# Performance work log

Measured on AMD Instinct MI355X. Metric: run time of the kernel, lower is better.

The kernel has to match this reference:

```python
import jax, jax.numpy as jnp
import numpy as np

B, N = 1, 768
C_S, C_Z, C_H, H, PQ, PV = 384, 128, 16, 12, 4, 8
INF, EPS = 1e5, 1e-8
SOFTPLUS_INV_1 = 0.541324854612918


def _quat_to_rot(q):
    # q: [..., 4] unit quaternions (w, x, y, z) -> [..., 3, 3]
    w, x, y, z = q[..., 0], q[..., 1], q[..., 2], q[..., 3]
    R = jnp.stack([
        1 - 2 * (y * y + z * z), 2 * (x * y - w * z), 2 * (x * z + w * y),
        2 * (x * y + w * z), 1 - 2 * (x * x + z * z), 2 * (y * z - w * x),
        2 * (x * z - w * y), 2 * (y * z + w * x), 1 - 2 * (x * x + y * y),
    ], axis=-1)
    return R.reshape(q.shape[:-1] + (3, 3))


def setup_inputs() -> dict:
    key = jax.random.key(0)
    ks = jax.random.split(key, 24)
    def lin(k, din, dout):
        return jax.random.normal(k, (din, dout), jnp.float32) / np.sqrt(din)
    quat = jax.random.normal(ks[2], (B, N, 4), jnp.float32)
    quat = quat / jnp.linalg.norm(quat, axis=-1, keepdims=True)
    return {
        "s": jax.random.normal(ks[0], (B, N, C_S), jnp.float32),
        "z": jax.random.normal(ks[1], (B, N, N, C_Z), jnp.float32),
        "rot": _quat_to_rot(quat),
        "trans": 10.0 * jax.random.normal(ks[3], (B, N, 3), jnp.float32),
        "mask": jnp.ones((B, N), jnp.float32),
        "wq": lin(ks[4], C_S, H * C_H), "bq": jnp.zeros((H * C_H,), jnp.float32),
        "wkv": lin(ks[5], C_S, 2 * H * C_H), "bkv": jnp.zeros((2 * H * C_H,), jnp.float32),
        "wqp": lin(ks[6], C_S, H * PQ * 3), "bqp": jnp.zeros((H * PQ * 3,), jnp.float32),
        "wkvp": lin(ks[7], C_S, H * (PQ + PV) * 3), "bkvp": jnp.zeros((H * (PQ + PV) * 3,), jnp.float32),
        "wb": lin(ks[8], C_Z, H), "bb": jnp.zeros((H,), jnp.float32),
        "wdz": lin(ks[9], C_Z, C_Z // 4), "bdz": jnp.zeros((C_Z // 4,), jnp.float32),
        "head_weights": jnp.full((H,), SOFTPLUS_INV_1, jnp.float32),
        "wout": lin(ks[10], H * (C_Z // 4 + C_H + PV * 4), C_S),
        "bout": jnp.zeros((C_S,), jnp.float32),
    }


def reference(s, z, rot, trans, mask, wq, bq, wkv, bkv, wqp, bqp, wkvp, bkvp,
              wb, bb, wdz, bdz, head_weights, wout, bout):
    # scalar q, k, v: [B, N, H, C_H]
    q = (s @ wq + bq).reshape(B, N, H, C_H)
    kv = (s @ wkv + bkv).reshape(B, N, H, 2 * C_H)
    k, v = kv[..., :C_H], kv[..., C_H:]

    def make_pts(w, b, npts):
        p = s @ w + b                                       # [B, N, H*npts*3]
        p = jnp.stack(jnp.split(p, 3, axis=-1), axis=-1)    # [B, N, H*npts, 3]
        p = jnp.einsum('bnxy,bnpy->bnpx', rot, p) + trans[:, :, None, :]
        return p.reshape(B, N, H, npts, 3)

    q_pts = make_pts(wqp, bqp, PQ)                          # [B, N, H, PQ, 3]
    kv_pts = make_pts(wkvp, bkvp, PQ + PV)
    k_pts, v_pts = kv_pts[..., :PQ, :], kv_pts[..., PQ:, :]

    b_bias = z @ wb + bb                                    # [B, N, N, H]
    a = jnp.einsum('bihc,bjhc->bhij', q, k) * np.sqrt(1.0 / (3 * C_H))
    a = a + np.sqrt(1.0 / 3) * jnp.transpose(b_bias, (0, 3, 1, 2))

    disp = q_pts[:, :, None] - k_pts[:, None]               # [B, i, j, H, PQ, 3]
    pt_att = jnp.sum(disp ** 2, axis=-1)                    # [B, i, j, H, PQ]
    hw = jax.nn.softplus(head_weights) * np.sqrt(1.0 / (3 * (PQ * 9.0 / 2)))
    pt_att = -0.5 * jnp.sum(pt_att * hw[:, None], axis=-1)  # [B, i, j, H]
    a = a + jnp.transpose(pt_att, (0, 3, 1, 2))

    sq_mask = INF * (mask[:, :, None] * mask[:, None, :] - 1.0)
    a = jax.nn.softmax(a + sq_mask[:, None], axis=-1)       # [B, H, i, j]

    o = jnp.einsum('bhij,bjhc->bihc', a, v).reshape(B, N, -1)
    o_pt = jnp.einsum('bhij,bjhpx->bihpx', a, v_pts)        # [B, N, H, PV, 3]
    o_pt = jnp.einsum('bixy,bihpx->bihpy', rot, o_pt - trans[:, :, None, None, :])
    o_pt_norm = jnp.sqrt(jnp.sum(o_pt ** 2, axis=-1) + EPS).reshape(B, N, -1)
    o_pt = o_pt.reshape(B, N, -1, 3)

    pair_z = z @ wdz + bdz                                  # [B, N, N, C_Z//4]
    o_pair = jnp.einsum('bhij,bijc->bihc', a, pair_z).reshape(B, N, -1)

    feats = jnp.concatenate(
        [o, o_pt[..., 0], o_pt[..., 1], o_pt[..., 2], o_pt_norm, o_pair], axis=-1)
    return feats @ wout + bout
```

## Files before the change

kernel.cpp:

```cpp
#include <hip/hip_runtime.h>
#include <hip/hip_bf16.h>
#include <math.h>

#define NTOK 768
#define CS   384
#define CZ   128
#define NH   12
#define INF_ 100000.0f
#define EPS_ 1e-8f

typedef unsigned int  uint32;
typedef __attribute__((ext_vector_type(8))) short bf16x8;
typedef __attribute__((ext_vector_type(4))) float f32x4;

__device__ __forceinline__ float bflo(uint32 u) { return __uint_as_float((u & 0xffffu) << 16); }
__device__ __forceinline__ float bfhi(uint32 u) { return __uint_as_float(u & 0xffff0000u); }
__device__ __forceinline__ uint32 pkbf(float a, float b) {
    union { unsigned short s[2]; uint32 u; } r;
    __hip_bfloat16 ha = __float2bfloat16(a);
    __hip_bfloat16 hb = __float2bfloat16(b);
    __builtin_memcpy(&r.s[0], &ha, 2);
    __builtin_memcpy(&r.s[1], &hb, 2);
    return r.u;
}

#define QK_SCALE 0.14433756729740643f
#define B_SCALE  0.5773502691896258f
#define HW_SCALE 0.13608276348795434f

__global__ __launch_bounds__(256) void k1a_gemm(
    const float* __restrict__ s,
    const float* __restrict__ wq, const float* __restrict__ wkv,
    const float* __restrict__ wqp, const float* __restrict__ wkvp,
    float* __restrict__ RAW)
{
    __shared__ float sA[32][72];
    __shared__ float sB[32][72];
    const int tid  = threadIdx.x;
    const int tok0 = blockIdx.x * 64;
    const int col0 = blockIdx.y * 64;

    const int m0 = (tid & 15) * 4;
    const int n0 = (tid >> 4) * 4;

    float4 acc[4];
    #pragma unroll
    for (int nn = 0; nn < 4; nn++) acc[nn] = make_float4(0.f, 0.f, 0.f, 0.f);

    const int lam = tid >> 2, lak = (tid & 3) * 8;
    const int lbk = tid >> 3, lbc = (tid & 7) * 8;
    const int gcol = col0 + lbc;
    const float* wsrc; int wwidth, woff;
    if (gcol < 192)      { wsrc = wq;   wwidth = 192; woff = gcol; }
    else if (gcol < 576) { wsrc = wkv;  wwidth = 384; woff = gcol - 192; }
    else if (gcol < 720) { wsrc = wqp;  wwidth = 144; woff = gcol - 576; }
    else                 { wsrc = wkvp; wwidth = 432; woff = gcol - 720; }

    for (int kb = 0; kb < CS; kb += 32) {
        const float4 a0 = *(const float4*)&s[(tok0 + lam) * CS + kb + lak];
        const float4 a1 = *(const float4*)&s[(tok0 + lam) * CS + kb + lak + 4];
        const float4 b0 = *(const float4*)&wsrc[(size_t)(kb + lbk) * wwidth + woff];
        const float4 b1 = *(const float4*)&wsrc[(size_t)(kb + lbk) * wwidth + woff + 4];
        __syncthreads();
        sA[lak + 0][lam] = a0.x; sA[lak + 1][lam] = a0.y;
        sA[lak + 2][lam] = a0.z; sA[lak + 3][lam] = a0.w;
        sA[lak + 4][lam] = a1.x; sA[lak + 5][lam] = a1.y;
        sA[lak + 6][lam] = a1.z; sA[lak + 7][lam] = a1.w;
        *(float4*)&sB[lbk][lbc]     = b0;
        *(float4*)&sB[lbk][lbc + 4] = b1;
        __syncthreads();
        #pragma unroll
        for (int k = 0; k < 32; k++) {
            const float4 av = *(const float4*)&sA[k][m0];
            const float4 bv = *(const float4*)&sB[k][n0];
            acc[0].x += av.x * bv.x; acc[0].y += av.y * bv.x; acc[0].z += av.z * bv.x; acc[0].w += av.w * bv.x;
            acc[1].x += av.x * bv.y; acc[1].y += av.y * bv.y; acc[1].z += av.z * bv.y; acc[1].w += av.w * bv.y;
            acc[2].x += av.x * bv.z; acc[2].y += av.y * bv.z; acc[2].z += av.z * bv.z; acc[2].w += av.w * bv.z;
            acc[3].x += av.x * bv.w; acc[3].y += av.y * bv.w; acc[3].z += av.z * bv.w; acc[3].w += av.w * bv.w;
        }
    }
    #pragma unroll
    for (int nn = 0; nn < 4; nn++)
        *(float4*)&RAW[(size_t)(col0 + n0 + nn) * NTOK + tok0 + m0] = acc[nn];
}

__global__ __launch_bounds__(256) void k1b_finish(
    const float* __restrict__ RAW,
    const float* __restrict__ rot, const float* __restrict__ trans,
    const float* __restrict__ bq, const float* __restrict__ bkv,
    const float* __restrict__ bqp, const float* __restrict__ bkvp,
    const float* __restrict__ head_weights,
    float* __restrict__ VT, float* __restrict__ QP, float* __restrict__ VPT,
    float* __restrict__ AP, float* __restrict__ BP,
    float* __restrict__ RQN, float* __restrict__ CKN)
{
    __shared__ float hwS[NH];
    const int tid = threadIdx.x;
    const int t  = blockIdx.x * 16 + (tid & 15);
    const int wk = tid >> 4;

    if (tid < NH) hwS[tid] = logf(1.0f + expf(head_weights[tid])) * HW_SCALE;

    float R[9], T3[3];
    #pragma unroll
    for (int x = 0; x < 9; x++) R[x] = rot[t * 9 + x];
    #pragma unroll
    for (int x = 0; x < 3; x++) T3[x] = trans[t * 3 + x];
    __syncthreads();

    for (int col = wk; col < 192; col += 16) {
        const int h = col >> 4, c = col & 15;
        AP[(size_t)(h * 28 + c) * NTOK + t] = QK_SCALE * (RAW[(size_t)col * NTOK + t] + bq[col]);
    }
    for (int idx = wk; idx < 192; idx += 16) {
        const int h = idx >> 4, c = idx & 15;
        BP[(size_t)(h * 28 + c) * NTOK + t] = RAW[(size_t)(192 + h * 32 + c) * NTOK + t] + bkv[h * 32 + c];
        VT[idx * NTOK + t] = RAW[(size_t)(192 + h * 32 + 16 + c) * NTOK + t] + bkv[h * 32 + 16 + c];
    }
    for (int pidx = wk; pidx < 48; pidx += 16) {
        const int h = pidx >> 2, p = pidx & 3;
        const float r0 = RAW[(size_t)(576 + 0 * 48 + pidx) * NTOK + t] + bqp[0 * 48 + pidx];
        const float r1 = RAW[(size_t)(576 + 1 * 48 + pidx) * NTOK + t] + bqp[1 * 48 + pidx];
        const float r2 = RAW[(size_t)(576 + 2 * 48 + pidx) * NTOK + t] + bqp[2 * 48 + pidx];
        #pragma unroll
        for (int x = 0; x < 3; x++) {
            const float v = R[x*3+0]*r0 + R[x*3+1]*r1 + R[x*3+2]*r2 + T3[x];
            QP[t * 144 + pidx * 3 + x] = v;
            AP[(size_t)(h * 28 + 16 + p * 3 + x) * NTOK + t] = hwS[h] * v;
        }
    }
    for (int pidx = wk; pidx < 144; pidx += 16) {
        const int h = pidx / 12, pp = pidx % 12;
        const float r0 = RAW[(size_t)(720 + 0 * 144 + pidx) * NTOK + t] + bkvp[0 * 144 + pidx];
        const float r1 = RAW[(size_t)(720 + 1 * 144 + pidx) * NTOK + t] + bkvp[1 * 144 + pidx];
        const float r2 = RAW[(size_t)(720 + 2 * 144 + pidx) * NTOK + t] + bkvp[2 * 144 + pidx];
        #pragma unroll
        for (int x = 0; x < 3; x++) {
            const float v = R[x*3+0]*r0 + R[x*3+1]*r1 + R[x*3+2]*r2 + T3[x];
            if (pp < 4) BP[(size_t)(h * 28 + 16 + pp * 3 + x) * NTOK + t] = v;
            else        VPT[((h * 8 + pp - 4) * 3 + x) * NTOK + t] = v;
        }
    }
    __syncthreads();
    if (wk < NH) {
        const int h = wk;
        float sq = 0.f, sk = 0.f;
        #pragma unroll
        for (int d = 0; d < 12; d++) {
            const float a = QP[t * 144 + h * 12 + d];
            sq += a * a;
            const float b = BP[(size_t)(h * 28 + 16 + d) * NTOK + t];
            sk += b * b;
        }
        RQN[h * NTOK + t] = -0.5f * hwS[h] * sq;
        CKN[h * NTOK + t] = -0.5f * hwS[h] * sk;
    }
}

__global__ __launch_bounds__(256) void k2_zproj_mfma(
    const float* __restrict__ z, const float* __restrict__ wb, const float* __restrict__ bb,
    const float* __restrict__ wdz, const float* __restrict__ bdz,
    float* __restrict__ BBT, uint32* __restrict__ PZB)
{
    __shared__ __align__(16) unsigned short wB[48 * 136];
    __shared__ float outS[2][64][53];
    __shared__ float bbS[12], bdzS[32];

    const int tid = threadIdx.x;
    const int i   = blockIdx.x;
    const int l   = tid & 63;
    const int jt  = tid >> 6;

    for (int idx = tid; idx < 48 * 64; idx += 256) {
        const int o = idx >> 6, k2 = (idx & 63) * 2;
        float f0, f1;
        if (o < 12)      { f0 = wb[k2 * 12 + o];         f1 = wb[(k2 + 1) * 12 + o]; }
        else if (o < 44) { f0 = wdz[k2 * 32 + (o - 12)]; f1 = wdz[(k2 + 1) * 32 + (o - 12)]; }
        else             { f0 = 0.f; f1 = 0.f; }
        *(uint32*)&wB[o * 136 + k2] = pkbf(f0, f1);
    }
    if (tid < 12) bbS[tid] = bb[tid];
    else if (tid >= 32 && tid < 64) bdzS[tid - 32] = bdz[tid - 32];
    __syncthreads();

    bf16x8 Bf[3][4];
    #pragma unroll
    for (int t = 0; t < 3; t++)
        #pragma unroll
        for (int ks = 0; ks < 4; ks++)
            Bf[t][ks] = *(const bf16x8*)&wB[(t * 16 + (l & 15)) * 136 + ks * 32 + (l >> 4) * 8];

    const float* zb = z + ((size_t)i * NTOK + jt * 16 + (l & 15)) * CZ + (l >> 4) * 8;

    float4 pa[8];
    #pragma unroll
    for (int ks = 0; ks < 4; ks++) {
        pa[2 * ks]     = *(const float4*)&zb[ks * 32];
        pa[2 * ks + 1] = *(const float4*)&zb[ks * 32 + 4];
    }

    for (int tile = 0; tile < 12; tile++) {
        const int j0  = tile * 64;
        const int buf = tile & 1;

        union { uint32 u[4]; bf16x8 v; } Au[4];
        #pragma unroll
        for (int ks = 0; ks < 4; ks++) {
            Au[ks].u[0] = pkbf(pa[2 * ks].x,     pa[2 * ks].y);
            Au[ks].u[1] = pkbf(pa[2 * ks].z,     pa[2 * ks].w);
            Au[ks].u[2] = pkbf(pa[2 * ks + 1].x, pa[2 * ks + 1].y);
            Au[ks].u[3] = pkbf(pa[2 * ks + 1].z, pa[2 * ks + 1].w);
        }
        if (tile < 11) {
            const float* zn = zb + (size_t)(tile + 1) * 64 * CZ;
            #pragma unroll
            for (int ks = 0; ks < 4; ks++) {
                pa[2 * ks]     = *(const float4*)&zn[ks * 32];
                pa[2 * ks + 1] = *(const float4*)&zn[ks * 32 + 4];
            }
        }

        f32x4 acc[3];
        #pragma unroll
        for (int t = 0; t < 3; t++) acc[t] = (f32x4){0.f, 0.f, 0.f, 0.f};
        #pragma unroll
        for (int ks = 0; ks < 4; ks++)
            #pragma unroll
            for (int t = 0; t < 3; t++)
                acc[t] = __builtin_amdgcn_mfma_f32_16x16x32_bf16(Au[ks].v, Bf[t][ks], acc[t], 0, 0, 0);

        #pragma unroll
        for (int t = 0; t < 3; t++) {
            const int o = t * 16 + (l & 15);
            #pragma unroll
            for (int v = 0; v < 4; v++)
                outS[buf][jt * 16 + (l >> 4) * 4 + v][o] = acc[t][v];
        }
        __syncthreads();

        for (int idx = tid; idx < 12 * 64; idx += 256) {
            const int o = idx >> 6, jl = idx & 63;
            BBT[((size_t)i * 12 + o) * NTOK + j0 + jl] = outS[buf][jl][o] + bbS[o];
        }
        for (int idx = tid; idx < 32 * 32; idx += 256) {
            const int c = idx >> 5, jp = idx & 31;
            const float f0 = outS[buf][jp * 2][12 + c] + bdzS[c];
            const float f1 = outS[buf][jp * 2 + 1][12 + c] + bdzS[c];
            PZB[(size_t)(i * 32 + c) * 384 + (j0 >> 1) + jp] = pkbf(f0, f1);
        }
    }
}

__global__ __launch_bounds__(768) void k3_fused(
    const float* __restrict__ AP, const float* __restrict__ BP,
    const float* __restrict__ RQN, const float* __restrict__ CKN,
    const float* __restrict__ BBT, const float* __restrict__ mask,
    const float* __restrict__ VT, const float* __restrict__ VPT,
    const uint32* __restrict__ PZB,
    float* __restrict__ O, float* __restrict__ OPT, float* __restrict__ OPAIR)
{
    const int i = blockIdx.x, tid = threadIdx.x;
    const int h = tid >> 6, l = tid & 63;

    float ap[28];
    #pragma unroll
    for (int k = 0; k < 28; k++) ap[k] = AP[(size_t)(h * 28 + k) * NTOK + i];
    const float rq = RQN[h * NTOK + i];
    const float mi = mask[i];

    f32x4 lg[3];
    #pragma unroll
    for (int qb = 0; qb < 3; qb++) {
        const int j4 = qb * 256 + l * 4;
        const float4 ck  = *(const float4*)&CKN[h * NTOK + j4];
        const float4 bbv = *(const float4*)&BBT[((size_t)i * 12 + h) * NTOK + j4];
        const float4 mj  = *(const float4*)&mask[j4];
        f32x4 a;
        a[0] = B_SCALE * bbv.x + rq + ck.x + INF_ * (mi * mj.x - 1.0f);
        a[1] = B_SCALE * bbv.y + rq + ck.y + INF_ * (mi * mj.y - 1.0f);
        a[2] = B_SCALE * bbv.z + rq + ck.z + INF_ * (mi * mj.z - 1.0f);
        a[3] = B_SCALE * bbv.w + rq + ck.w + INF_ * (mi * mj.w - 1.0f);
        #pragma unroll
        for (int k = 0; k < 28; k++) {
            const float4 bp = *(const float4*)&BP[(size_t)(h * 28 + k) * NTOK + j4];
            a[0] += ap[k] * bp.x; a[1] += ap[k] * bp.y;
            a[2] += ap[k] * bp.z; a[3] += ap[k] * bp.w;
        }
        lg[qb] = a;
    }

    float m = -3.0e38f;
    #pragma unroll
    for (int qb = 0; qb < 3; qb++)
        #pragma unroll
        for (int v = 0; v < 4; v++) m = fmaxf(m, lg[qb][v]);
    #pragma unroll
    for (int off = 32; off >= 1; off >>= 1) m = fmaxf(m, __shfl_xor(m, off));
    float ssum = 0.0f;
    #pragma unroll
    for (int qb = 0; qb < 3; qb++)
        #pragma unroll
        for (int v = 0; v < 4; v++) {
            const float e = __expf(lg[qb][v] - m);
            lg[qb][v] = e;
            ssum += e;
        }
    #pragma unroll
    for (int off = 32; off >= 1; off >>= 1) ssum += __shfl_xor(ssum, off);
    const float inv = 1.0f / ssum;
    #pragma unroll
    for (int qb = 0; qb < 3; qb++)
        #pragma unroll
        for (int v = 0; v < 4; v++) lg[qb][v] *= inv;

    #pragma unroll 2
    for (int r = 0; r < 40; r++) {
        const float4* src = (r < 16) ? (const float4*)&VT[(h * 16 + r) * NTOK]
                                     : (const float4*)&VPT[(h * 24 + (r - 16)) * NTOK];
        const float4 v0 = src[l], v1 = src[64 + l], v2 = src[128 + l];
        float acc = lg[0][0]*v0.x + lg[0][1]*v0.y + lg[0][2]*v0.z + lg[0][3]*v0.w
                  + lg[1][0]*v1.x + lg[1][1]*v1.y + lg[1][2]*v1.z + lg[1][3]*v1.w
                  + lg[2][0]*v2.x + lg[2][1]*v2.y + lg[2][2]*v2.z + lg[2][3]*v2.w;
        #pragma unroll
        for (int off = 32; off >= 1; off >>= 1) acc += __shfl_xor(acc, off);
        if (l == 0) {
            if (r < 16) O[i * 192 + h * 16 + r] = acc;
            else        OPT[i * 288 + h * 24 + (r - 16)] = acc;
        }
    }
    #pragma unroll 2
    for (int c = 0; c < 32; c++) {
        const uint2* src = (const uint2*)PZB + (size_t)(i * 32 + c) * 192;
        float a = 0.f;
        #pragma unroll
        for (int it = 0; it < 3; it++) {
            const uint2 u = src[it * 64 + l];
            a += lg[it][0] * bflo(u.x) + lg[it][1] * bfhi(u.x)
               + lg[it][2] * bflo(u.y) + lg[it][3] * bfhi(u.y);
        }
        #pragma unroll
        for (int off = 32; off >= 1; off >>= 1) a += __shfl_xor(a, off);
        if (l == 0) OPAIR[i * 384 + h * 32 + c] = a;
    }
}

#define K4T 8
__global__ __launch_bounds__(256) void k4_out(
    const float* __restrict__ O, const float* __restrict__ OPT, const float* __restrict__ OPAIR,
    const float* __restrict__ rot, const float* __restrict__ trans,
    const float* __restrict__ wout, const float* __restrict__ bout,
    float* __restrict__ out)
{
    __shared__ float f[K4T][960];
    const int n0 = blockIdx.x * K4T, tid = threadIdx.x;

    for (int idx = tid; idx < K4T * 192; idx += 256) {
        const int t = idx / 192, k = idx % 192;
        f[t][k] = O[(n0 + t) * 192 + k];
    }
    for (int idx = tid; idx < K4T * 384; idx += 256) {
        const int t = idx / 384, k = idx % 384;
        f[t][576 + k] = OPAIR[(n0 + t) * 384 + k];
    }
    for (int idx = tid; idx < K4T * 96; idx += 256) {
        const int t = idx / 96, hp = idx % 96;
        const int n = n0 + t;
        const float vx = OPT[n * 288 + hp * 3 + 0] - trans[n * 3 + 0];
        const float vy = OPT[n * 288 + hp * 3 + 1] - trans[n * 3 + 1];
        const float vz = OPT[n * 288 + hp * 3 + 2] - trans[n * 3 + 2];
        const float o0 = rot[n*9+0]*vx + rot[n*9+3]*vy + rot[n*9+6]*vz;
        const float o1 = rot[n*9+1]*vx + rot[n*9+4]*vy + rot[n*9+7]*vz;
        const float o2 = rot[n*9+2]*vx + rot[n*9+5]*vy + rot[n*9+8]*vz;
        f[t][192 + hp] = o0;
        f[t][288 + hp] = o1;
        f[t][384 + hp] = o2;
        f[t][480 + hp] = sqrtf(o0*o0 + o1*o1 + o2*o2 + EPS_);
    }
    __syncthreads();

    for (int o = tid; o < 384; o += 256) {
        float acc[K4T];
        #pragma unroll
        for (int t = 0; t < K4T; t++) acc[t] = bout[o];
        for (int kq = 0; kq < 240; kq++) {
            float4 fv[K4T];
            #pragma unroll
            for (int t = 0; t < K4T; t++) fv[t] = *(const float4*)&f[t][kq * 4];
            #pragma unroll
            for (int kk = 0; kk < 4; kk++) {
                const float wv = wout[(kq * 4 + kk) * 384 + o];
                #pragma unroll
                for (int t = 0; t < K4T; t++) {
                    const float fe = (kk == 0) ? fv[t].x : (kk == 1) ? fv[t].y
                                   : (kk == 2) ? fv[t].z : fv[t].w;
                    acc[t] += fe * wv;
                }
            }
        }
        #pragma unroll
        for (int t = 0; t < K4T; t++) out[(n0 + t) * 384 + o] = acc[t];
    }
}

extern "C" void kernel_launch(void* const* d_in, const int* in_sizes, int n_in,
                              void* d_out, int out_size, void* d_ws, size_t ws_size,
                              hipStream_t stream) {
    (void)in_sizes; (void)n_in; (void)out_size; (void)ws_size;
    const float* s     = (const float*)d_in[0];
    const float* z     = (const float*)d_in[1];
    const float* rot   = (const float*)d_in[2];
    const float* trans = (const float*)d_in[3];
    const float* mask  = (const float*)d_in[4];
    const float* wq    = (const float*)d_in[5];
    const float* bq    = (const float*)d_in[6];
    const float* wkv   = (const float*)d_in[7];
    const float* bkv   = (const float*)d_in[8];
    const float* wqp   = (const float*)d_in[9];
    const float* bqp   = (const float*)d_in[10];
    const float* wkvp  = (const float*)d_in[11];
    const float* bkvp  = (const float*)d_in[12];
    const float* wb    = (const float*)d_in[13];
    const float* bb    = (const float*)d_in[14];
    const float* wdz   = (const float*)d_in[15];
    const float* bdz   = (const float*)d_in[16];
    const float* hwts  = (const float*)d_in[17];
    const float* wout  = (const float*)d_in[18];
    const float* bout  = (const float*)d_in[19];
    float* out = (float*)d_out;

    float* ws = (float*)d_ws;
    float* Q     = ws;
    float* KT    = Q     + 147456;
    float* VT    = KT    + 147456;
    float* QP    = VT    + 147456;
    float* KPT   = QP    + 110592;
    float* VPT   = KPT   + 110592;
    float* O     = VPT   + 221184;
    float* OPT   = O     + 147456;
    float* OPAIR = OPT   + 221184;
    float* BBT   = OPAIR + 294912;
    uint32* PZB  = (uint32*)(BBT + 7077888);
    float* AP    = BBT + 7077888 + 9437184;
    float* BP    = AP  + 258048;
    float* RQN   = BP  + 258048;
    float* CKN   = RQN + 9216;
    float* RAW = BBT;

    hipLaunchKernelGGL(k1a_gemm, dim3(NTOK / 64, 1152 / 64), dim3(256), 0, stream,
                       s, wq, wkv, wqp, wkvp, RAW);
    hipLaunchKernelGGL(k1b_finish, dim3(NTOK / 16), dim3(256), 0, stream,
                       RAW, rot, trans, bq, bkv, bqp, bkvp, hwts,
                       VT, QP, VPT, AP, BP, RQN, CKN);
    hipLaunchKernelGGL(k2_zproj_mfma, dim3(NTOK), dim3(256), 0, stream,
                       z, wb, bb, wdz, bdz, BBT, PZB);
    hipLaunchKernelGGL(k3_fused, dim3(NTOK), dim3(768), 0, stream,
                       AP, BP, RQN, CKN, BBT, mask, VT, VPT, PZB,
                       O, OPT, OPAIR);
    hipLaunchKernelGGL(k4_out, dim3(NTOK / K4T), dim3(256), 0, stream,
                       O, OPT, OPAIR, rot, trans, wout, bout, out);
}
```

Before: 383.9 us.

## Fuse z-projection into attention kernel, keeping pair bias and pair values in LDS

New measurement: 329.0 us. 1.17x faster.

```diff
diff --git a/kernel.cpp b/kernel.cpp
--- a/kernel.cpp
+++ b/kernel.cpp
@@ -157,27 +157,31 @@
     }
 }
 
-__global__ __launch_bounds__(256) void k2_zproj_mfma(
+__global__ __launch_bounds__(768) void k23_fused(
     const float* __restrict__ z, const float* __restrict__ wb, const float* __restrict__ bb,
     const float* __restrict__ wdz, const float* __restrict__ bdz,
-    float* __restrict__ BBT, uint32* __restrict__ PZB)
+    const float* __restrict__ AP, const float* __restrict__ BP,
+    const float* __restrict__ RQN, const float* __restrict__ CKN,
+    const float* __restrict__ mask,
+    const float* __restrict__ VT, const float* __restrict__ VPT,
+    float* __restrict__ O, float* __restrict__ OPT, float* __restrict__ OPAIR)
 {
-    __shared__ __align__(16) unsigned short wB[48 * 136];
-    __shared__ float outS[2][64][53];
+    __shared__ __align__(16) unsigned short wBs[48 * 136];
+    __shared__ float  bbL[12][772];
+    __shared__ uint32 pzL[32][386];
     __shared__ float bbS[12], bdzS[32];
 
-    const int tid = threadIdx.x;
-    const int i   = blockIdx.x;
-    const int l   = tid & 63;
-    const int jt  = tid >> 6;
-
-    for (int idx = tid; idx < 48 * 64; idx += 256) {
+    const int i = blockIdx.x, tid = threadIdx.x;
+    const int h = tid >> 6;
+    const int l = tid & 63;
+
+    for (int idx = tid; idx < 48 * 64; idx += 768) {
         const int o = idx >> 6, k2 = (idx & 63) * 2;
         float f0, f1;
         if (o < 12)      { f0 = wb[k2 * 12 + o];         f1 = wb[(k2 + 1) * 12 + o]; }
         else if (o < 44) { f0 = wdz[k2 * 32 + (o - 12)]; f1 = wdz[(k2 + 1) * 32 + (o - 12)]; }
         else             { f0 = 0.f; f1 = 0.f; }
-        *(uint32*)&wB[o * 136 + k2] = pkbf(f0, f1);
+        *(uint32*)&wBs[o * 136 + k2] = pkbf(f0, f1);
     }
     if (tid < 12) bbS[tid] = bb[tid];
     else if (tid >= 32 && tid < 64) bdzS[tid - 32] = bdz[tid - 32];
@@ -188,10 +192,9 @@
     for (int t = 0; t < 3; t++)
         #pragma unroll
         for (int ks = 0; ks < 4; ks++)
-            Bf[t][ks] = *(const bf16x8*)&wB[(t * 16 + (l & 15)) * 136 + ks * 32 + (l >> 4) * 8];
-
-    const float* zb = z + ((size_t)i * NTOK + jt * 16 + (l & 15)) * CZ + (l >> 4) * 8;
-
+            Bf[t][ks] = *(const bf16x8*)&wBs[(t * 16 + (l & 15)) * 136 + ks * 32 + (l >> 4) * 8];
+
+    const float* zb = z + ((size_t)i * NTOK + h * 64 + (l & 15)) * CZ + (l >> 4) * 8;
     float4 pa[8];
     #pragma unroll
     for (int ks = 0; ks < 4; ks++) {
@@ -199,10 +202,9 @@
         pa[2 * ks + 1] = *(const float4*)&zb[ks * 32 + 4];
     }
 
-    for (int tile = 0; tile < 12; tile++) {
-        const int j0  = tile * 64;
-        const int buf = tile & 1;
-
+    #pragma unroll
+    for (int st = 0; st < 4; st++) {
+        const int jb = h * 64 + st * 16;
         union { uint32 u[4]; bf16x8 v; } Au[4];
         #pragma unroll
         for (int ks = 0; ks < 4; ks++) {
@@ -211,8 +213,8 @@
             Au[ks].u[2] = pkbf(pa[2 * ks + 1].x, pa[2 * ks + 1].y);
             Au[ks].u[3] = pkbf(pa[2 * ks + 1].z, pa[2 * ks + 1].w);
         }
-        if (tile < 11) {
-            const float* zn = zb + (size_t)(tile + 1) * 64 * CZ;
+        if (st < 3) {
+            const float* zn = zb + (size_t)(st + 1) * 16 * CZ;
             #pragma unroll
             for (int ks = 0; ks < 4; ks++) {
                 pa[2 * ks]     = *(const float4*)&zn[ks * 32];
@@ -229,38 +231,23 @@
             for (int t = 0; t < 3; t++)
                 acc[t] = __builtin_amdgcn_mfma_f32_16x16x32_bf16(Au[ks].v, Bf[t][ks], acc[t], 0, 0, 0);
 
+        const int jq = jb + (l >> 4) * 4;
         #pragma unroll
         for (int t = 0; t < 3; t++) {
             const int o = t * 16 + (l & 15);
-            #pragma unroll
-            for (int v = 0; v < 4; v++)
-                outS[buf][jt * 16 + (l >> 4) * 4 + v][o] = acc[t][v];
-        }
-        __syncthreads();
-
-        for (int idx = tid; idx < 12 * 64; idx += 256) {
-            const int o = idx >> 6, jl = idx & 63;
-            BBT[((size_t)i * 12 + o) * NTOK + j0 + jl] = outS[buf][jl][o] + bbS[o];
-        }
-        for (int idx = tid; idx < 32 * 32; idx += 256) {
-            const int c = idx >> 5, jp = idx & 31;
-            const float f0 = outS[buf][jp * 2][12 + c] + bdzS[c];
-            const float f1 = outS[buf][jp * 2 + 1][12 + c] + bdzS[c];
-            PZB[(size_t)(i * 32 + c) * 384 + (j0 >> 1) + jp] = pkbf(f0, f1);
-        }
-    }
-}
-
-__global__ __launch_bounds__(768) void k3_fused(
-    const float* __restrict__ AP, const float* __restrict__ BP,
-    const float* __restrict__ RQN, const float* __restrict__ CKN,
-    const float* __restrict__ BBT, const float* __restrict__ mask,
-    const float* __restrict__ VT, const float* __restrict__ VPT,
-    const uint32* __restrict__ PZB,
-    float* __restrict__ O, float* __restrict__ OPT, float* __restrict__ OPAIR)
-{
-    const int i = blockIdx.x, tid = threadIdx.x;
-    const int h = tid >> 6, l = tid & 63;
+            if (o < 12) {
+                #pragma unroll
+                for (int v = 0; v < 4; v++)
+                    bbL[o][jq + v] = acc[t][v] + bbS[o];
+            } else if (o < 44) {
+                const int c = o - 12;
+                const float bz = bdzS[c];
+                pzL[c][(jq >> 1)]     = pkbf(acc[t][0] + bz, acc[t][1] + bz);
+                pzL[c][(jq >> 1) + 1] = pkbf(acc[t][2] + bz, acc[t][3] + bz);
+            }
+        }
+    }
+    __syncthreads();
 
     float ap[28];
     #pragma unroll
@@ -273,7 +260,7 @@
     for (int qb = 0; qb < 3; qb++) {
         const int j4 = qb * 256 + l * 4;
         const float4 ck  = *(const float4*)&CKN[h * NTOK + j4];
-        const float4 bbv = *(const float4*)&BBT[((size_t)i * 12 + h) * NTOK + j4];
+        const float4 bbv = *(const float4*)&bbL[h][j4];
         const float4 mj  = *(const float4*)&mask[j4];
         f32x4 a;
         a[0] = B_SCALE * bbv.x + rq + ck.x + INF_ * (mi * mj.x - 1.0f);
@@ -330,13 +317,13 @@
     }
     #pragma unroll 2
     for (int c = 0; c < 32; c++) {
-        const uint2* src = (const uint2*)PZB + (size_t)(i * 32 + c) * 192;
         float a = 0.f;
         #pragma unroll
         for (int it = 0; it < 3; it++) {
-            const uint2 u = src[it * 64 + l];
-            a += lg[it][0] * bflo(u.x) + lg[it][1] * bfhi(u.x)
-               + lg[it][2] * bflo(u.y) + lg[it][3] * bfhi(u.y);
+            const uint32* p2 = &pzL[c][it * 128 + 2 * l];
+            const uint32 ux = p2[0], uy = p2[1];
+            a += lg[it][0] * bflo(ux) + lg[it][1] * bfhi(ux)
+               + lg[it][2] * bflo(uy) + lg[it][3] * bfhi(uy);
         }
         #pragma unroll
         for (int off = 32; off >= 1; off >>= 1) a += __shfl_xor(a, off);
@@ -438,23 +425,20 @@
     float* O     = VPT   + 221184;
     float* OPT   = O     + 147456;
     float* OPAIR = OPT   + 221184;
-    float* BBT   = OPAIR + 294912;
-    uint32* PZB  = (uint32*)(BBT + 7077888);
-    float* AP    = BBT + 7077888 + 9437184;
+    float* RAW   = OPAIR + 294912;
+    float* AP    = RAW   + 884736;
     float* BP    = AP  + 258048;
     float* RQN   = BP  + 258048;
     float* CKN   = RQN + 9216;
-    float* RAW = BBT;
 
     hipLaunchKernelGGL(k1a_gemm, dim3(NTOK / 64, 1152 / 64), dim3(256), 0, stream,
                        s, wq, wkv, wqp, wkvp, RAW);
     hipLaunchKernelGGL(k1b_finish, dim3(NTOK / 16), dim3(256), 0, stream,
                        RAW, rot, trans, bq, bkv, bqp, bkvp, hwts,
                        VT, QP, VPT, AP, BP, RQN, CKN);
-    hipLaunchKernelGGL(k2_zproj_mfma, dim3(NTOK), dim3(256), 0, stream,
-                       z, wb, bb, wdz, bdz, BBT, PZB);
-    hipLaunchKernelGGL(k3_fused, dim3(NTOK), dim3(768), 0, stream,
-                       AP, BP, RQN, CKN, BBT, mask, VT, VPT, PZB,
+    hipLaunchKernelGGL(k23_fused, dim3(NTOK), dim3(768), 0, stream,
+                       z, wb, bb, wdz, bdz,
+                       AP, BP, RQN, CKN, mask, VT, VPT,
                        O, OPT, OPAIR);
     hipLaunchKernelGGL(k4_out, dim3(NTOK / K4T), dim3(256), 0, stream,
                        O, OPT, OPAIR, rot, trans, wout, bout, out);
```
